# Kernel optimization log

Hardware: AMD Instinct MI355X
Metric: run time of the kernel (lower is better)

## Reference

```python
import jax, jax.numpy as jnp
import numpy as np

B, T, U, H = 16, 256, 96, 512


def setup_inputs() -> dict:
    key = jax.random.key(0)
    k1, k2, k3, k4 = jax.random.split(key, 4)
    f = jax.random.normal(k1, (B, T, H), dtype=jnp.float32)
    g = jax.random.normal(k2, (B, U, H), dtype=jnp.float32)
    f_len = jax.random.randint(k3, (B,), 1, T + 1, dtype=jnp.int32)
    g_len = jax.random.randint(k4, (B,), 1, U + 1, dtype=jnp.int32)
    return {"f": f, "g": g, "f_len": f_len, "g_len": g_len}


def reference(f, g, f_len, g_len):
    # f: (B, T, H), g: (B, U, H) -> h: (B, T, U, H)
    # h[b,t,u,:] = f[b,t,:] + g[b,u,:] for t < f_len[b], u < g_len[b]; else 0.
    Bc, Tc, Hc = f.shape
    Uc = g.shape[1]
    t_valid = jnp.arange(Tc)[None, :] < f_len[:, None]          # (B, T)
    u_valid = jnp.arange(Uc)[None, :] < g_len[:, None]          # (B, U)
    mask = (t_valid[:, :, None] & u_valid[:, None, :])[..., None]  # (B, T, U, 1)
    h = f[:, :, None, :] + g[:, None, :, :]                     # (B, T, U, H)
    return jnp.where(mask, h, jnp.zeros((), dtype=f.dtype))
```

## Files before the change

### kernel.cpp

```cpp
#include <hip/hip_runtime.h>
#include <hip/hip_bf16.h>


#define TJ_B 16
#define TJ_T 256
#define TJ_U 96
#define TJ_H4 128
#define TJ_TT 2
#define TJ_NTH 512
#define TJ_K ((TJ_U * TJ_H4) / TJ_NTH)

typedef float fx4 __attribute__((ext_vector_type(4)));

__global__ __launch_bounds__(TJ_NTH) void TransducerJoint_66915590472509_kernel(
    const fx4* __restrict__ f,
    const fx4* __restrict__ g,
    const int* __restrict__ f_len,
    const int* __restrict__ g_len,
    fx4* __restrict__ out)
{
    const int bid = blockIdx.x;
    const int b   = bid >> 7;
    const int t0  = (bid & 127) * TJ_TT;
    const int i   = threadIdx.x;
    const int h4  = i & (TJ_H4 - 1);
    const int uu  = i >> 7;

    const int flen = f_len[b];
    const int glen = g_len[b];

    fx4 fr[TJ_TT];
    #pragma unroll
    for (int tt = 0; tt < TJ_TT; ++tt)
        fr[tt] = f[(size_t)(b * TJ_T + t0 + tt) * TJ_H4 + h4];

    fx4 gr[TJ_K];
    const fx4* gb = g + (size_t)b * (TJ_U * TJ_H4);
    #pragma unroll
    for (int k = 0; k < TJ_K; ++k)
        gr[k] = gb[i + TJ_NTH * k];

    #pragma unroll
    for (int tt = 0; tt < TJ_TT; ++tt) {
        const int t = t0 + tt;
        const bool tok = (t < flen);
        const fx4 fv = fr[tt];
        fx4* op = out + (size_t)(b * TJ_T + t) * (TJ_U * TJ_H4) + i;
        #pragma unroll
        for (int k = 0; k < TJ_K; ++k) {
            const bool ok = tok && ((uu + 4 * k) < glen);
            op[TJ_NTH * k] = ok ? (fv + gr[k]) : (fx4)0.f;
        }
    }
}

extern "C" void kernel_launch(void* const* d_in, const int* in_sizes, int n_in,
                              void* d_out, int out_size, void* d_ws, size_t ws_size,
                              hipStream_t stream) {
    const fx4* f     = (const fx4*)d_in[0];
    const fx4* g     = (const fx4*)d_in[1];
    const int* f_len = (const int*)d_in[2];
    const int* g_len = (const int*)d_in[3];
    fx4*       out   = (fx4*)d_out;

    const int nblocks = TJ_B * (TJ_T / TJ_TT);
    TransducerJoint_66915590472509_kernel<<<nblocks, TJ_NTH, 0, stream>>>(
        f, g, f_len, g_len, out);
}
```

Measured before the change: 794.1 us.

## Persistent-style blocks with double-buffered f/g chunk loads overlapping stores

Reduces the grid from 2048 to 512 blocks, so each block handles 8 timesteps of one batch in 12 chunks (4 t-pairs × 3 u-segments). The loads for the next chunk go into a second register buffer while the current chunk is stored, so load latency overlaps the streaming writes. The output is write-bandwidth bound (about 200 MB), so any gain would come from latency hiding and fewer block launches. The cost is more registers for the double buffer and less parallelism at the block level.

```diff
diff --git a/kernel.cpp b/kernel.cpp
--- a/kernel.cpp
+++ b/kernel.cpp
@@ -2,17 +2,14 @@
 #include <hip/hip_bf16.h>
 
 
-#define TJ_B 16
 #define TJ_T 256
 #define TJ_U 96
 #define TJ_H4 128
-#define TJ_TT 2
-#define TJ_NTH 512
-#define TJ_K ((TJ_U * TJ_H4) / TJ_NTH)
+#define TJ_ROW (TJ_U * TJ_H4)
 
 typedef float fx4 __attribute__((ext_vector_type(4)));
 
-__global__ __launch_bounds__(TJ_NTH) void TransducerJoint_66915590472509_kernel(
+__global__ __launch_bounds__(512) void TransducerJoint_66915590472509_kernel(
     const fx4* __restrict__ f,
     const fx4* __restrict__ g,
     const int* __restrict__ f_len,
@@ -20,8 +17,8 @@
     fx4* __restrict__ out)
 {
     const int bid = blockIdx.x;
-    const int b   = bid >> 7;
-    const int t0  = (bid & 127) * TJ_TT;
+    const int b   = bid >> 5;
+    const int tc0 = (bid & 31) << 2;
     const int i   = threadIdx.x;
     const int h4  = i & (TJ_H4 - 1);
     const int uu  = i >> 7;
@@ -29,27 +26,71 @@
     const int flen = f_len[b];
     const int glen = g_len[b];
 
-    fx4 fr[TJ_TT];
+    const fx4* fb = f + (size_t)b * TJ_T * TJ_H4;
+    const fx4* gb = g + (size_t)b * TJ_ROW;
+    fx4*       ob = out + (size_t)b * TJ_T * TJ_ROW;
+
+    fx4 ga[2][8];
+    fx4 fa[2][2];
+
+    #define TJ_LOADC(buf, c)                                                  \
+        do {                                                                  \
+            constexpr int j_ = (c) / 3, r_ = (c) - 3 * ((c) / 3);             \
+            const int t0_ = (tc0 + j_) * 2;                                   \
+            fa[buf][0] = fb[(t0_ + 0) * TJ_H4 + h4];                          \
+            fa[buf][1] = fb[(t0_ + 1) * TJ_H4 + h4];                          \
+            _Pragma("unroll")                                                 \
+            for (int k = 0; k < 8; ++k)                                       \
+                ga[buf][k] = gb[r_ * 4096 + i + 512 * k];                     \
+        } while (0)
+
+    #define TJ_STOREC(buf, c)                                                 \
+        do {                                                                  \
+            constexpr int j_ = (c) / 3, r_ = (c) - 3 * ((c) / 3);             \
+            const int t0_ = (tc0 + j_) * 2;                                   \
+            _Pragma("unroll")                                                 \
+            for (int tt = 0; tt < 2; ++tt) {                                  \
+                const bool tok_ = (t0_ + tt) < flen;                          \
+                const fx4 fv_ = fa[buf][tt];                                  \
+                fx4* op_ = ob + (size_t)(t0_ + tt) * TJ_ROW + r_ * 4096 + i;  \
+                _Pragma("unroll")                                             \
+                for (int k = 0; k < 8; ++k) {                                 \
+                    const bool ok_ = tok_ && (r_ * 32 + uu + 4 * k) < glen;   \
+                    op_[512 * k] = ok_ ? (fv_ + ga[buf][k]) : (fx4)0.f;       \
+                }                                                             \
+            }                                                                 \
+        } while (0)
+
+    TJ_LOADC(0, 0);
     #pragma unroll
-    for (int tt = 0; tt < TJ_TT; ++tt)
-        fr[tt] = f[(size_t)(b * TJ_T + t0 + tt) * TJ_H4 + h4];
-
-    fx4 gr[TJ_K];
-    const fx4* gb = g + (size_t)b * (TJ_U * TJ_H4);
-    #pragma unroll
-    for (int k = 0; k < TJ_K; ++k)
-        gr[k] = gb[i + TJ_NTH * k];
-
-    #pragma unroll
-    for (int tt = 0; tt < TJ_TT; ++tt) {
-        const int t = t0 + tt;
-        const bool tok = (t < flen);
-        const fx4 fv = fr[tt];
-        fx4* op = out + (size_t)(b * TJ_T + t) * (TJ_U * TJ_H4) + i;
-        #pragma unroll
-        for (int k = 0; k < TJ_K; ++k) {
-            const bool ok = tok && ((uu + 4 * k) < glen);
-            op[TJ_NTH * k] = ok ? (fv + gr[k]) : (fx4)0.f;
+    for (int c = 0; c < 12; ++c) {
+        switch (c + 1) {
+            case 1:  TJ_LOADC(1, 1);  break;
+            case 2:  TJ_LOADC(0, 2);  break;
+            case 3:  TJ_LOADC(1, 3);  break;
+            case 4:  TJ_LOADC(0, 4);  break;
+            case 5:  TJ_LOADC(1, 5);  break;
+            case 6:  TJ_LOADC(0, 6);  break;
+            case 7:  TJ_LOADC(1, 7);  break;
+            case 8:  TJ_LOADC(0, 8);  break;
+            case 9:  TJ_LOADC(1, 9);  break;
+            case 10: TJ_LOADC(0, 10); break;
+            case 11: TJ_LOADC(1, 11); break;
+            default: break;
+        }
+        switch (c) {
+            case 0:  TJ_STOREC(0, 0);  break;
+            case 1:  TJ_STOREC(1, 1);  break;
+            case 2:  TJ_STOREC(0, 2);  break;
+            case 3:  TJ_STOREC(1, 3);  break;
+            case 4:  TJ_STOREC(0, 4);  break;
+            case 5:  TJ_STOREC(1, 5);  break;
+            case 6:  TJ_STOREC(0, 6);  break;
+            case 7:  TJ_STOREC(1, 7);  break;
+            case 8:  TJ_STOREC(0, 8);  break;
+            case 9:  TJ_STOREC(1, 9);  break;
+            case 10: TJ_STOREC(0, 10); break;
+            case 11: TJ_STOREC(1, 11); break;
         }
     }
 }
@@ -63,7 +104,6 @@
     const int* g_len = (const int*)d_in[3];
     fx4*       out   = (fx4*)d_out;
 
-    const int nblocks = TJ_B * (TJ_T / TJ_TT);
-    TransducerJoint_66915590472509_kernel<<<nblocks, TJ_NTH, 0, stream>>>(
+    TransducerJoint_66915590472509_kernel<<<512, 512, 0, stream>>>(
         f, g, f_len, g_len, out);
 }
```

New measurement: 796.2 us. No clear change (+0.3%).
